# Performance work log

Measured on AMD Instinct MI355X. Metric: run time of the kernel, lower is better.

## Reference

```python
import jax, jax.numpy as jnp
import numpy as np

B, Q, H = 8, 4, 4096
NH, NKV, HD = 32, 8, 128
G = NH // NKV          # GQA group size
S = 4096               # tokens already in KV cache
CAP = S + Q            # cache capacity
SCALE = 1.0 / (HD ** 0.5)
ROPE_BASE = 10000.0


def setup_inputs() -> dict:
    key = jax.random.key(0)
    ks = jax.random.split(key, 8)
    hidden_states = jax.random.normal(ks[0], (B, Q, H), jnp.float32) * 0.02
    cache_lens = jnp.full((B,), S, dtype=jnp.int32)
    # rope tables for the new token positions [cache_len, cache_len+Q)
    pos = (cache_lens[:, None] + jnp.arange(Q)[None, :]).astype(jnp.float32)  # [B,Q]
    inv_freq = 1.0 / (ROPE_BASE ** (jnp.arange(0, HD, 2, dtype=jnp.float32) / HD))
    freqs = pos[..., None] * inv_freq[None, None, :]        # [B,Q,HD/2]
    emb = jnp.concatenate([freqs, freqs], axis=-1)          # [B,Q,HD]
    cos, sin = jnp.cos(emb), jnp.sin(emb)
    w_scale = H ** -0.5
    Wq = jax.random.normal(ks[1], (H, NH * HD), jnp.float32) * w_scale
    Wk = jax.random.normal(ks[2], (H, NKV * HD), jnp.float32) * w_scale
    Wv = jax.random.normal(ks[3], (H, NKV * HD), jnp.float32) * w_scale
    Wo = jax.random.normal(ks[4], (NH * HD, H), jnp.float32) * w_scale
    K_cache = jax.random.normal(ks[5], (B, CAP, NKV, HD), jnp.float32) * 0.02
    V_cache = jax.random.normal(ks[6], (B, CAP, NKV, HD), jnp.float32) * 0.02
    return dict(hidden_states=hidden_states, cos=cos, sin=sin,
                Wq=Wq, Wk=Wk, Wv=Wv, Wo=Wo,
                K_cache=K_cache, V_cache=V_cache, cache_lens=cache_lens)


def _rotate_half(x):
    x1, x2 = jnp.split(x, 2, axis=-1)
    return jnp.concatenate([-x2, x1], axis=-1)


def reference(hidden_states, cos, sin, Wq, Wk, Wv, Wo, K_cache, V_cache, cache_lens):
    # QKV projections (bias-free, Llama style)
    q = (hidden_states @ Wq).reshape(B, Q, NH, HD)
    k = (hidden_states @ Wk).reshape(B, Q, NKV, HD)
    v = (hidden_states @ Wv).reshape(B, Q, NKV, HD)
    # RoPE (unsqueeze_dim=2 -> broadcast over heads)
    c, s = cos[:, :, None, :], sin[:, :, None, :]
    q = q * c + _rotate_half(q) * s
    k = k * c + _rotate_half(k) * s
    # write new K/V into cache at position cache_lens (per batch)
    b_idx = jnp.arange(B)[:, None]                         # [B,1]
    w_idx = cache_lens[:, None] + jnp.arange(Q)[None, :]   # [B,Q]
    K = K_cache.at[b_idx, w_idx].set(k)                    # [B,CAP,NKV,HD]
    V = V_cache.at[b_idx, w_idx].set(v)
    # GQA attention without materializing repeated KV
    qg = q.reshape(B, Q, NKV, G, HD)
    scores = jnp.einsum('bqkgd,bskd->bkgqs', qg, K) * SCALE  # [B,NKV,G,Q,CAP]
    # causal mask: query i sees cache positions <= cache_lens + i
    j = jnp.arange(CAP)
    valid = j[None, None, :] <= (cache_lens[:, None, None] + jnp.arange(Q)[None, :, None])  # [B,Q,CAP]
    scores = jnp.where(valid[:, None, None, :, :], scores, -jnp.inf)
    p = jax.nn.softmax(scores, axis=-1)
    o = jnp.einsum('bkgqs,bskd->bqkgd', p, V).reshape(B, Q, NH * HD)
    return o @ Wo
```

## Files before the change

### kernel.cpp

```cpp
#include <hip/hip_runtime.h>
#include <hip/hip_bf16.h>

#define BB 8
#define QQ 4
#define HH 4096
#define NH 32
#define NKV 8
#define GG 4
#define HD 128
#define SS 4096
#define CAP 4100
#define ROWS 32
#define NQCOL 4096
#define NKCOL 1024
#define NTOTC 6144
#define KSPLIT 32
#define KCHUNK 128
#define SCALE 0.08838834764831845f
#define TS 128
#define NSPLIT 33
#define NEG_BIG 1e30f

__global__ __launch_bounds__(256) void gemm32_part(
    const float* __restrict__ x, const float* __restrict__ W0,
    const float* __restrict__ W1, const float* __restrict__ W2,
    int n0, int n01, int ntot, float* __restrict__ part) {
  int nblk = ntot >> 8;
  int cb = blockIdx.x % nblk;
  int kb = blockIdx.x / nblk;
  int c = (cb << 8) + threadIdx.x;
  int k0 = kb << 7;

  const float* W;
  int ldw, wc;
  if (c < n0)       { W = W0; ldw = n0;         wc = c; }
  else if (c < n01) { W = W1; ldw = n01 - n0;   wc = c - n0; }
  else              { W = W2; ldw = ntot - n01; wc = c - n01; }

  const float* wp = W + (size_t)k0 * ldw + wc;
  const float* xp = x + k0;

  float acc[ROWS];
#pragma unroll
  for (int r = 0; r < ROWS; ++r) acc[r] = 0.f;

  float w0 = wp[0], w1 = wp[ldw], w2 = wp[2 * ldw], w3 = wp[3 * ldw];
  for (int kk = 0; kk < KCHUNK; kk += 4) {
    int adv = (kk + 4 < KCHUNK) ? (ldw << 2) : 0;
    wp += adv;
    float n0r = wp[0], n1r = wp[ldw], n2r = wp[2 * ldw], n3r = wp[3 * ldw];
#pragma unroll
    for (int r = 0; r < ROWS; ++r) {
      const float4 xv = *(const float4*)(xp + (r << 12) + kk);
      acc[r] = fmaf(xv.x, w0, acc[r]);
      acc[r] = fmaf(xv.y, w1, acc[r]);
      acc[r] = fmaf(xv.z, w2, acc[r]);
      acc[r] = fmaf(xv.w, w3, acc[r]);
    }
    w0 = n0r; w1 = n1r; w2 = n2r; w3 = n3r;
  }
#pragma unroll
  for (int r = 0; r < ROWS; ++r) part[(size_t)((kb << 5) + r) * ntot + c] = acc[r];
}

__global__ __launch_bounds__(256) void rope_reduce_scatter(
    const float* __restrict__ ypart, const float* __restrict__ cosb,
    const float* __restrict__ sinb, const int* __restrict__ cache_lens,
    float* __restrict__ q_buf, float* __restrict__ K_cache,
    float* __restrict__ V_cache) {
  int idx = blockIdx.x * 256 + threadIdx.x;
  if (idx < 81920) {
    int r = idx / 2560;
    int o = idx % 2560;
    int b = r >> 2, qp = r & 3;
    int c1, d;
    bool is_q;
    if (o < 2048) {
      int h = o >> 6; d = o & 63;
      c1 = h * HD + d;
      is_q = true;
    } else {
      int ok = o - 2048;
      int kvh = ok >> 6; d = ok & 63;
      c1 = NQCOL + kvh * HD + d;
      is_q = false;
    }
    int c2 = c1 + 64;
    float s1 = 0.f, s2 = 0.f;
#pragma unroll
    for (int kb = 0; kb < KSPLIT; ++kb) {
      s1 += ypart[(size_t)((kb << 5) + r) * NTOTC + c1];
      s2 += ypart[(size_t)((kb << 5) + r) * NTOTC + c2];
    }
    float cv = cosb[(r << 7) + d];
    float sv = sinb[(r << 7) + d];
    float o1 = s1 * cv - s2 * sv;
    float o2 = s2 * cv + s1 * sv;
    if (is_q) {
      q_buf[(size_t)r * NQCOL + c1] = o1 * SCALE;
      q_buf[(size_t)r * NQCOL + c2] = o2 * SCALE;
    } else {
      int kvh = (c1 - NQCOL) >> 7;
      int pos = cache_lens[b] + qp;
      size_t base = ((size_t)(b * CAP + pos) * NKV + kvh) * HD;
      K_cache[base + d] = o1;
      K_cache[base + d + 64] = o2;
    }
  } else {
    int vi = idx - 81920;
    int r = vi >> 10;
    int cc = vi & 1023;
    int b = r >> 2, qp = r & 3;
    int c = NQCOL + NKCOL + cc;
    float s = 0.f;
#pragma unroll
    for (int kb = 0; kb < KSPLIT; ++kb)
      s += ypart[(size_t)((kb << 5) + r) * NTOTC + c];
    int kvh = cc >> 7, dd = cc & 127;
    int pos = cache_lens[b] + qp;
    V_cache[((size_t)(b * CAP + pos) * NKV + kvh) * HD + dd] = s;
  }
}

__global__ __launch_bounds__(256) void attn_partial(
    const float* __restrict__ q_buf, const float* __restrict__ K_cache,
    const float* __restrict__ V_cache, const int* __restrict__ cache_lens,
    float* __restrict__ part_o, float* __restrict__ part_m,
    float* __restrict__ part_l) {
  __shared__ __align__(16) float k_lds[64 * 128];
  __shared__ __align__(16) float q_lds[16 * 132];
  __shared__ __align__(16) float p_lds[64 * 20];
  __shared__ float ml_lds[32];
  __shared__ float alpha_lds[16];

  int g = blockIdx.x & 63;
  int split = blockIdx.x >> 6;
  int b = g >> 3, kv = g & 7;
  int t = threadIdx.x, w = t >> 6, lane = t & 63;
  int cl = cache_lens[b];
  int cl3 = cl + 3;
  int jb = split * TS;

  for (int i = t; i < 512; i += 256) {
    int qi = i >> 5, d4 = (i & 31) << 2;
    const float4 v = *(const float4*)(q_buf +
        (size_t)((b << 2) + (qi >> 2)) * NQCOL + (((kv << 2) + (qi & 3)) << 7) + d4);
    *(float4*)&q_lds[qi * 132 + d4] = v;
  }
  if (t < 16) { ml_lds[t] = -NEG_BIG; ml_lds[16 + t] = 0.f; }

  int pg = lane >> 2, dq = lane & 3;
  int dg = lane & 31, qh = lane >> 5;

  float orun[4][8];
#pragma unroll
  for (int di = 0; di < 4; ++di)
#pragma unroll
    for (int qq = 0; qq < 8; ++qq) orun[di][qq] = 0.f;

  for (int h = 0; h < 2; ++h) {
    int jbh = jb + (h << 6);

    for (int i = t; i < 2048; i += 256) {
      int r = i >> 5;
      int cbyte = (i & 31) << 4;
      int j = min(jbh + r, cl3);
      const float4 vv = *(const float4*)((const char*)K_cache +
          (((size_t)(b * CAP + j) * NKV + kv) << 9) + cbyte);
      *(float4*)((char*)k_lds + ((size_t)r << 9) + (cbyte ^ ((r & 7) << 4))) = vv;
    }
    __syncthreads();

    float acc[4][4];
#pragma unroll
    for (int i = 0; i < 4; ++i)
#pragma unroll
      for (int j = 0; j < 4; ++j) acc[i][j] = 0.f;

    for (int s = 0; s < 8; ++s) {
      int d0 = (dq << 5) + (s << 2);
      const float4 q0 = *(const float4*)&q_lds[(4 * w + 0) * 132 + d0];
      const float4 q1 = *(const float4*)&q_lds[(4 * w + 1) * 132 + d0];
      const float4 q2 = *(const float4*)&q_lds[(4 * w + 2) * 132 + d0];
      const float4 q3 = *(const float4*)&q_lds[(4 * w + 3) * 132 + d0];
#pragma unroll
      for (int i = 0; i < 4; ++i) {
        int r = pg + (i << 4);
        const float4 kk = *(const float4*)((const char*)k_lds +
            (r << 9) + ((unsigned)(d0 << 2) ^ ((r & 7) << 4)));
        acc[i][0] = fmaf(kk.x, q0.x, acc[i][0]);
        acc[i][0] = fmaf(kk.y, q0.y, acc[i][0]);
        acc[i][0] = fmaf(kk.z, q0.z, acc[i][0]);
        acc[i][0] = fmaf(kk.w, q0.w, acc[i][0]);
        acc[i][1] = fmaf(kk.x, q1.x, acc[i][1]);
        acc[i][1] = fmaf(kk.y, q1.y, acc[i][1]);
        acc[i][1] = fmaf(kk.z, q1.z, acc[i][1]);
        acc[i][1] = fmaf(kk.w, q1.w, acc[i][1]);
        acc[i][2] = fmaf(kk.x, q2.x, acc[i][2]);
        acc[i][2] = fmaf(kk.y, q2.y, acc[i][2]);
        acc[i][2] = fmaf(kk.z, q2.z, acc[i][2]);
        acc[i][2] = fmaf(kk.w, q2.w, acc[i][2]);
        acc[i][3] = fmaf(kk.x, q3.x, acc[i][3]);
        acc[i][3] = fmaf(kk.y, q3.y, acc[i][3]);
        acc[i][3] = fmaf(kk.z, q3.z, acc[i][3]);
        acc[i][3] = fmaf(kk.w, q3.w, acc[i][3]);
      }
    }

#pragma unroll
    for (int i = 0; i < 4; ++i)
#pragma unroll
      for (int j = 0; j < 4; ++j) {
        float v = acc[i][j];
        v += __shfl_xor(v, 1);
        v += __shfl_xor(v, 2);
        acc[i][j] = v;
      }

    bool okv[4];
#pragma unroll
    for (int i = 0; i < 4; ++i) {
      okv[i] = (jbh + pg + (i << 4)) <= (cl + w);
#pragma unroll
      for (int j = 0; j < 4; ++j)
        if (!okv[i]) acc[i][j] = -NEG_BIG;
    }

    float m4[4], l4[4], a4[4];
#pragma unroll
    for (int j = 0; j < 4; ++j) {
      float m = fmaxf(fmaxf(acc[0][j], acc[1][j]), fmaxf(acc[2][j], acc[3][j]));
      m = fmaxf(m, __shfl_xor(m, 4));
      m = fmaxf(m, __shfl_xor(m, 8));
      m = fmaxf(m, __shfl_xor(m, 16));
      m = fmaxf(m, __shfl_xor(m, 32));
      float mo = ml_lds[(w << 2) + j];
      float lo = ml_lds[16 + (w << 2) + j];
      float nm = fmaxf(mo, m);
      float l = 0.f;
#pragma unroll
      for (int i = 0; i < 4; ++i) {
        float e = okv[i] ? __expf(acc[i][j] - nm) : 0.f;
        acc[i][j] = e;
        l += e;
      }
      l += __shfl_xor(l, 4);
      l += __shfl_xor(l, 8);
      l += __shfl_xor(l, 16);
      l += __shfl_xor(l, 32);
      float al = __expf(mo - nm);
      m4[j] = nm; l4[j] = lo * al + l; a4[j] = al;
    }

#pragma unroll
    for (int i = 0; i < 4; ++i) {
      float pv = (dq == 0) ? acc[i][0] : (dq == 1) ? acc[i][1]
               : (dq == 2) ? acc[i][2] : acc[i][3];
      p_lds[(pg + (i << 4)) * 20 + (w << 2) + dq] = pv;
    }
    if (lane < 4) {
      float mm = (lane == 0) ? m4[0] : (lane == 1) ? m4[1] : (lane == 2) ? m4[2] : m4[3];
      float ll = (lane == 0) ? l4[0] : (lane == 1) ? l4[1] : (lane == 2) ? l4[2] : l4[3];
      float aa = (lane == 0) ? a4[0] : (lane == 1) ? a4[1] : (lane == 2) ? a4[2] : a4[3];
      ml_lds[(w << 2) + lane] = mm;
      ml_lds[16 + (w << 2) + lane] = ll;
      alpha_lds[(w << 2) + lane] = aa;
    }
    __syncthreads();

    float alq[8];
#pragma unroll
    for (int qq = 0; qq < 8; ++qq) alq[qq] = alpha_lds[(qh << 3) + qq];
#pragma unroll
    for (int di = 0; di < 4; ++di)
#pragma unroll
      for (int qq = 0; qq < 8; ++qq) orun[di][qq] *= alq[qq];

    for (int jj = 0; jj < 16; ++jj) {
      int j = (w << 4) + jj;
      int jg = min(jbh + j, cl3);
      const float4 vv = *(const float4*)(V_cache +
          (((size_t)(b * CAP + jg) * NKV + kv) << 7) + (dg << 2));
      const float4 pa = *(const float4*)&p_lds[j * 20 + (qh << 3)];
      const float4 pb = *(const float4*)&p_lds[j * 20 + (qh << 3) + 4];
      orun[0][0] = fmaf(vv.x, pa.x, orun[0][0]); orun[1][0] = fmaf(vv.y, pa.x, orun[1][0]);
      orun[2][0] = fmaf(vv.z, pa.x, orun[2][0]); orun[3][0] = fmaf(vv.w, pa.x, orun[3][0]);
      orun[0][1] = fmaf(vv.x, pa.y, orun[0][1]); orun[1][1] = fmaf(vv.y, pa.y, orun[1][1]);
      orun[2][1] = fmaf(vv.z, pa.y, orun[2][1]); orun[3][1] = fmaf(vv.w, pa.y, orun[3][1]);
      orun[0][2] = fmaf(vv.x, pa.z, orun[0][2]); orun[1][2] = fmaf(vv.y, pa.z, orun[1][2]);
      orun[2][2] = fmaf(vv.z, pa.z, orun[2][2]); orun[3][2] = fmaf(vv.w, pa.z, orun[3][2]);
      orun[0][3] = fmaf(vv.x, pa.w, orun[0][3]); orun[1][3] = fmaf(vv.y, pa.w, orun[1][3]);
      orun[2][3] = fmaf(vv.z, pa.w, orun[2][3]); orun[3][3] = fmaf(vv.w, pa.w, orun[3][3]);
      orun[0][4] = fmaf(vv.x, pb.x, orun[0][4]); orun[1][4] = fmaf(vv.y, pb.x, orun[1][4]);
      orun[2][4] = fmaf(vv.z, pb.x, orun[2][4]); orun[3][4] = fmaf(vv.w, pb.x, orun[3][4]);
      orun[0][5] = fmaf(vv.x, pb.y, orun[0][5]); orun[1][5] = fmaf(vv.y, pb.y, orun[1][5]);
      orun[2][5] = fmaf(vv.z, pb.y, orun[2][5]); orun[3][5] = fmaf(vv.w, pb.y, orun[3][5]);
      orun[0][6] = fmaf(vv.x, pb.z, orun[0][6]); orun[1][6] = fmaf(vv.y, pb.z, orun[1][6]);
      orun[2][6] = fmaf(vv.z, pb.z, orun[2][6]); orun[3][6] = fmaf(vv.w, pb.z, orun[3][6]);
      orun[0][7] = fmaf(vv.x, pb.w, orun[0][7]); orun[1][7] = fmaf(vv.y, pb.w, orun[1][7]);
      orun[2][7] = fmaf(vv.z, pb.w, orun[2][7]); orun[3][7] = fmaf(vv.w, pb.w, orun[3][7]);
    }
  }

  float* om = k_lds;
#pragma unroll
  for (int qq = 0; qq < 8; ++qq) {
    int q = (qh << 3) + qq;
    float4 ov = make_float4(orun[0][qq], orun[1][qq], orun[2][qq], orun[3][qq]);
    *(float4*)&om[(size_t)(((w << 4) + q) << 7) + (dg << 2)] = ov;
  }
  __syncthreads();

  size_t ob = (size_t)(split * 64 + g) * 2048;
  for (int i = t; i < 2048; i += 256)
    part_o[ob + i] = om[i] + om[i + 2048] + om[i + 4096] + om[i + 6144];
  if (t < 16) {
    part_m[(size_t)(split * 64 + g) * 16 + t] = ml_lds[t];
    part_l[(size_t)(split * 64 + g) * 16 + t] = ml_lds[16 + t];
  }
}

__global__ __launch_bounds__(256) void attn_combine(
    const float* __restrict__ part_o, const float* __restrict__ part_m,
    const float* __restrict__ part_l, float* __restrict__ attn_out) {
  int idx = blockIdx.x * 256 + threadIdx.x;
  int d = idx & 127;
  int qi = (idx >> 7) & 15;
  int g = idx >> 11;
  int b = g >> 3, kv = g & 7;
  float M = -NEG_BIG;
#pragma unroll 4
  for (int s = 0; s < NSPLIT; ++s) M = fmaxf(M, part_m[(size_t)(s * 64 + g) * 16 + qi]);
  float osum = 0.f, L = 0.f;
#pragma unroll 4
  for (int s = 0; s < NSPLIT; ++s) {
    size_t ml = (size_t)(s * 64 + g) * 16 + qi;
    float wgt = __expf(part_m[ml] - M);
    osum += part_o[ml * 128 + d] * wgt;
    L += part_l[ml] * wgt;
  }
  int qp = qi >> 2, gi = qi & 3;
  attn_out[(size_t)((b << 2) + qp) * NQCOL + (((kv << 2) + gi) << 7) + d] = osum / L;
}

__global__ __launch_bounds__(256) void reduce_out(
    const float* __restrict__ opart, float* __restrict__ out) {
  int idx = blockIdx.x * 256 + threadIdx.x;
  int c = idx & 4095;
  int r = idx >> 12;
  float s = 0.f;
#pragma unroll
  for (int kb = 0; kb < KSPLIT; ++kb)
    s += opart[(size_t)((kb << 5) + r) * NQCOL + c];
  out[idx] = s;
}

extern "C" void kernel_launch(void* const* d_in, const int* in_sizes, int n_in,
                              void* d_out, int out_size, void* d_ws, size_t ws_size,
                              hipStream_t stream) {
  const float* hidden = (const float*)d_in[0];
  const float* cosb   = (const float*)d_in[1];
  const float* sinb   = (const float*)d_in[2];
  const float* Wq     = (const float*)d_in[3];
  const float* Wk     = (const float*)d_in[4];
  const float* Wv     = (const float*)d_in[5];
  const float* Wo     = (const float*)d_in[6];
  float* K_cache      = (float*)d_in[7];
  float* V_cache      = (float*)d_in[8];
  const int* cache_lens = (const int*)d_in[9];
  float* out = (float*)d_out;

  const size_t BUF0 = (size_t)KSPLIT * ROWS * NTOTC;
  float* buf0     = (float*)d_ws;
  float* q_buf    = buf0 + BUF0;
  float* part_m   = q_buf + (size_t)ROWS * NQCOL;
  float* part_l   = part_m + (size_t)NSPLIT * 64 * 16;
  float* attn_out = part_l + (size_t)NSPLIT * 64 * 16;

  gemm32_part<<<(NTOTC / 256) * KSPLIT, 256, 0, stream>>>(
      hidden, Wq, Wk, Wv, NQCOL, NQCOL + NKCOL, NTOTC, buf0);
  rope_reduce_scatter<<<448, 256, 0, stream>>>(
      buf0, cosb, sinb, cache_lens, q_buf, K_cache, V_cache);
  attn_partial<<<64 * NSPLIT, 256, 0, stream>>>(
      q_buf, K_cache, V_cache, cache_lens, buf0, part_m, part_l);
  attn_combine<<<512, 256, 0, stream>>>(buf0, part_m, part_l, attn_out);
  gemm32_part<<<(NQCOL / 256) * KSPLIT, 256, 0, stream>>>(
      attn_out, Wo, Wo, Wo, NQCOL, NQCOL, NQCOL, buf0);
  reduce_out<<<512, 256, 0, stream>>>(buf0, out);
}
```

Before: 556.4 us.

## Stage activations in LDS, prefetch weights, and double-buffer K tiles in attention

```diff
diff --git a/kernel.cpp b/kernel.cpp
--- a/kernel.cpp
+++ b/kernel.cpp
@@ -6,9 +6,7 @@
 #define HH 4096
 #define NH 32
 #define NKV 8
-#define GG 4
 #define HD 128
-#define SS 4096
 #define CAP 4100
 #define ROWS 32
 #define NQCOL 4096
@@ -21,46 +19,114 @@
 #define NSPLIT 33
 #define NEG_BIG 1e30f
 
+template <bool WIDE>
 __global__ __launch_bounds__(256) void gemm32_part(
     const float* __restrict__ x, const float* __restrict__ W0,
     const float* __restrict__ W1, const float* __restrict__ W2,
     int n0, int n01, int ntot, float* __restrict__ part) {
-  int nblk = ntot >> 8;
+  __shared__ __align__(16) float x_lds[ROWS * KCHUNK];
+  const int CPB = WIDE ? 512 : 256;
+  int nblk = ntot / CPB;
   int cb = blockIdx.x % nblk;
   int kb = blockIdx.x / nblk;
-  int c = (cb << 8) + threadIdx.x;
   int k0 = kb << 7;
 
-  const float* W;
-  int ldw, wc;
+  for (int i = threadIdx.x; i < 1024; i += 256) {
+    int r = i >> 5, gq = (i & 31) << 2;
+    *(float4*)&x_lds[(r << 7) + gq] =
+        *(const float4*)(x + ((size_t)r << 12) + k0 + gq);
+  }
+  __syncthreads();
+
+  int c = cb * CPB + (WIDE ? (threadIdx.x << 1) : (int)threadIdx.x);
+  const float* W; int ldw, wc;
   if (c < n0)       { W = W0; ldw = n0;         wc = c; }
   else if (c < n01) { W = W1; ldw = n01 - n0;   wc = c - n0; }
   else              { W = W2; ldw = ntot - n01; wc = c - n01; }
-
   const float* wp = W + (size_t)k0 * ldw + wc;
-  const float* xp = x + k0;
-
-  float acc[ROWS];
-#pragma unroll
-  for (int r = 0; r < ROWS; ++r) acc[r] = 0.f;
-
-  float w0 = wp[0], w1 = wp[ldw], w2 = wp[2 * ldw], w3 = wp[3 * ldw];
-  for (int kk = 0; kk < KCHUNK; kk += 4) {
-    int adv = (kk + 4 < KCHUNK) ? (ldw << 2) : 0;
-    wp += adv;
-    float n0r = wp[0], n1r = wp[ldw], n2r = wp[2 * ldw], n3r = wp[3 * ldw];
+
+  if (WIDE) {
+    float acc[ROWS][2];
+#pragma unroll
+    for (int r = 0; r < ROWS; ++r) { acc[r][0] = 0.f; acc[r][1] = 0.f; }
+    float2 a[4], bq[4];
+#pragma unroll
+    for (int u = 0; u < 4; ++u) {
+      const float* p0 = wp + (size_t)u * ldw;
+      const float* p1 = wp + (size_t)(u + 4) * ldw;
+      a[u].x = __builtin_nontemporal_load(p0);
+      a[u].y = __builtin_nontemporal_load(p0 + 1);
+      bq[u].x = __builtin_nontemporal_load(p1);
+      bq[u].y = __builtin_nontemporal_load(p1 + 1);
+    }
+    for (int kk = 0; kk < KCHUNK; kk += 4) {
+      float2 cq[4];
+      if (kk + 8 < KCHUNK) {
+#pragma unroll
+        for (int u = 0; u < 4; ++u) {
+          const float* p = wp + (size_t)(kk + 8 + u) * ldw;
+          cq[u].x = __builtin_nontemporal_load(p);
+          cq[u].y = __builtin_nontemporal_load(p + 1);
+        }
+      } else {
+#pragma unroll
+        for (int u = 0; u < 4; ++u) cq[u] = a[u];
+      }
+#pragma unroll
+      for (int r = 0; r < ROWS; ++r) {
+        const float4 xv = *(const float4*)&x_lds[(r << 7) + kk];
+        acc[r][0] = fmaf(xv.x, a[0].x, acc[r][0]);
+        acc[r][1] = fmaf(xv.x, a[0].y, acc[r][1]);
+        acc[r][0] = fmaf(xv.y, a[1].x, acc[r][0]);
+        acc[r][1] = fmaf(xv.y, a[1].y, acc[r][1]);
+        acc[r][0] = fmaf(xv.z, a[2].x, acc[r][0]);
+        acc[r][1] = fmaf(xv.z, a[2].y, acc[r][1]);
+        acc[r][0] = fmaf(xv.w, a[3].x, acc[r][0]);
+        acc[r][1] = fmaf(xv.w, a[3].y, acc[r][1]);
+      }
+#pragma unroll
+      for (int u = 0; u < 4; ++u) { a[u] = bq[u]; bq[u] = cq[u]; }
+    }
 #pragma unroll
     for (int r = 0; r < ROWS; ++r) {
-      const float4 xv = *(const float4*)(xp + (r << 12) + kk);
-      acc[r] = fmaf(xv.x, w0, acc[r]);
-      acc[r] = fmaf(xv.y, w1, acc[r]);
-      acc[r] = fmaf(xv.z, w2, acc[r]);
-      acc[r] = fmaf(xv.w, w3, acc[r]);
-    }
-    w0 = n0r; w1 = n1r; w2 = n2r; w3 = n3r;
-  }
-#pragma unroll
-  for (int r = 0; r < ROWS; ++r) part[(size_t)((kb << 5) + r) * ntot + c] = acc[r];
+      float2 st = make_float2(acc[r][0], acc[r][1]);
+      *(float2*)(part + (size_t)((kb << 5) + r) * ntot + c) = st;
+    }
+  } else {
+    float acc[ROWS];
+#pragma unroll
+    for (int r = 0; r < ROWS; ++r) acc[r] = 0.f;
+    float a[4], bq[4];
+#pragma unroll
+    for (int u = 0; u < 4; ++u) {
+      a[u] = __builtin_nontemporal_load(wp + (size_t)u * ldw);
+      bq[u] = __builtin_nontemporal_load(wp + (size_t)(u + 4) * ldw);
+    }
+    for (int kk = 0; kk < KCHUNK; kk += 4) {
+      float cq[4];
+      if (kk + 8 < KCHUNK) {
+#pragma unroll
+        for (int u = 0; u < 4; ++u)
+          cq[u] = __builtin_nontemporal_load(wp + (size_t)(kk + 8 + u) * ldw);
+      } else {
+#pragma unroll
+        for (int u = 0; u < 4; ++u) cq[u] = a[u];
+      }
+#pragma unroll
+      for (int r = 0; r < ROWS; ++r) {
+        const float4 xv = *(const float4*)&x_lds[(r << 7) + kk];
+        acc[r] = fmaf(xv.x, a[0], acc[r]);
+        acc[r] = fmaf(xv.y, a[1], acc[r]);
+        acc[r] = fmaf(xv.z, a[2], acc[r]);
+        acc[r] = fmaf(xv.w, a[3], acc[r]);
+      }
+#pragma unroll
+      for (int u = 0; u < 4; ++u) { a[u] = bq[u]; bq[u] = cq[u]; }
+    }
+#pragma unroll
+    for (int r = 0; r < ROWS; ++r)
+      part[(size_t)((kb << 5) + r) * ntot + c] = acc[r];
+  }
 }
 
 __global__ __launch_bounds__(256) void rope_reduce_scatter(
@@ -127,9 +193,9 @@
     const float* __restrict__ V_cache, const int* __restrict__ cache_lens,
     float* __restrict__ part_o, float* __restrict__ part_m,
     float* __restrict__ part_l) {
-  __shared__ __align__(16) float k_lds[64 * 128];
-  __shared__ __align__(16) float q_lds[16 * 132];
-  __shared__ __align__(16) float p_lds[64 * 20];
+  __shared__ __align__(16) float k_lds[2][32 * 128];
+  __shared__ __align__(16) float q_lds[16 * 144];
+  __shared__ __align__(16) float p_lds[32 * 20];
   __shared__ float ml_lds[32];
   __shared__ float alpha_lds[16];
 
@@ -145,49 +211,78 @@
     int qi = i >> 5, d4 = (i & 31) << 2;
     const float4 v = *(const float4*)(q_buf +
         (size_t)((b << 2) + (qi >> 2)) * NQCOL + (((kv << 2) + (qi & 3)) << 7) + d4);
-    *(float4*)&q_lds[qi * 132 + d4] = v;
+    *(float4*)&q_lds[qi * 144 + (d4 >> 5) * 36 + (d4 & 31)] = v;
   }
   if (t < 16) { ml_lds[t] = -NEG_BIG; ml_lds[16 + t] = 0.f; }
 
   int pg = lane >> 2, dq = lane & 3;
   int dg = lane & 31, qh = lane >> 5;
 
+  float4 kreg[4];
+#pragma unroll
+  for (int u = 0; u < 4; ++u) {
+    int i = t + (u << 8);
+    int r = i >> 5, gk = i & 31;
+    int j = min(jb + r, cl3);
+    kreg[u] = *(const float4*)((const char*)K_cache +
+        (((size_t)(b * CAP + j) * NKV + kv) << 9) + (gk << 4));
+  }
+#pragma unroll
+  for (int u = 0; u < 4; ++u) {
+    int i = t + (u << 8);
+    int r = i >> 5, gk = i & 31;
+    *(float4*)((char*)&k_lds[0][0] + (r << 9) + ((gk << 4) ^ ((r & 7) << 4))) = kreg[u];
+  }
+  __syncthreads();
+
   float orun[4][8];
 #pragma unroll
   for (int di = 0; di < 4; ++di)
 #pragma unroll
     for (int qq = 0; qq < 8; ++qq) orun[di][qq] = 0.f;
 
-  for (int h = 0; h < 2; ++h) {
-    int jbh = jb + (h << 6);
-
-    for (int i = t; i < 2048; i += 256) {
-      int r = i >> 5;
-      int cbyte = (i & 31) << 4;
-      int j = min(jbh + r, cl3);
-      const float4 vv = *(const float4*)((const char*)K_cache +
-          (((size_t)(b * CAP + j) * NKV + kv) << 9) + cbyte);
-      *(float4*)((char*)k_lds + ((size_t)r << 9) + (cbyte ^ ((r & 7) << 4))) = vv;
-    }
-    __syncthreads();
-
-    float acc[4][4];
-#pragma unroll
-    for (int i = 0; i < 4; ++i)
+  int cur = 0;
+  for (int st = 0; st < 4; ++st) {
+    int jbh = jb + (st << 5);
+
+    float4 vreg[8];
+#pragma unroll
+    for (int jj = 0; jj < 8; ++jj) {
+      int j = min(jbh + (w << 3) + jj, cl3);
+      vreg[jj] = *(const float4*)(V_cache +
+          (((size_t)(b * CAP + j) * NKV + kv) << 7) + (dg << 2));
+    }
+    bool have_next = (st < 3);
+    if (have_next) {
+      int jbn = jbh + 32;
+#pragma unroll
+      for (int u = 0; u < 4; ++u) {
+        int i = t + (u << 8);
+        int r = i >> 5, gk = i & 31;
+        int j = min(jbn + r, cl3);
+        kreg[u] = *(const float4*)((const char*)K_cache +
+            (((size_t)(b * CAP + j) * NKV + kv) << 9) + (gk << 4));
+      }
+    }
+
+    const float* kl = &k_lds[cur][0];
+    float acc[2][4];
+#pragma unroll
+    for (int i = 0; i < 2; ++i)
 #pragma unroll
       for (int j = 0; j < 4; ++j) acc[i][j] = 0.f;
 
     for (int s = 0; s < 8; ++s) {
-      int d0 = (dq << 5) + (s << 2);
-      const float4 q0 = *(const float4*)&q_lds[(4 * w + 0) * 132 + d0];
-      const float4 q1 = *(const float4*)&q_lds[(4 * w + 1) * 132 + d0];
-      const float4 q2 = *(const float4*)&q_lds[(4 * w + 2) * 132 + d0];
-      const float4 q3 = *(const float4*)&q_lds[(4 * w + 3) * 132 + d0];
-#pragma unroll
-      for (int i = 0; i < 4; ++i) {
+      int qoff = dq * 36 + (s << 2);
+      const float4 q0 = *(const float4*)&q_lds[(4 * w + 0) * 144 + qoff];
+      const float4 q1 = *(const float4*)&q_lds[(4 * w + 1) * 144 + qoff];
+      const float4 q2 = *(const float4*)&q_lds[(4 * w + 2) * 144 + qoff];
+      const float4 q3 = *(const float4*)&q_lds[(4 * w + 3) * 144 + qoff];
+#pragma unroll
+      for (int i = 0; i < 2; ++i) {
         int r = pg + (i << 4);
-        const float4 kk = *(const float4*)((const char*)k_lds +
-            (r << 9) + ((unsigned)(d0 << 2) ^ ((r & 7) << 4)));
+        const float4 kk = *(const float4*)((const char*)kl +
+            (r << 9) + ((unsigned)((dq << 7) | (s << 4)) ^ ((r & 7) << 4)));
         acc[i][0] = fmaf(kk.x, q0.x, acc[i][0]);
         acc[i][0] = fmaf(kk.y, q0.y, acc[i][0]);
         acc[i][0] = fmaf(kk.z, q0.z, acc[i][0]);
@@ -208,7 +303,7 @@
     }
 
 #pragma unroll
-    for (int i = 0; i < 4; ++i)
+    for (int i = 0; i < 2; ++i)
 #pragma unroll
       for (int j = 0; j < 4; ++j) {
         float v = acc[i][j];
@@ -217,9 +312,9 @@
         acc[i][j] = v;
       }
 
-    bool okv[4];
-#pragma unroll
-    for (int i = 0; i < 4; ++i) {
+    bool okv[2];
+#pragma unroll
+    for (int i = 0; i < 2; ++i) {
       okv[i] = (jbh + pg + (i << 4)) <= (cl + w);
 #pragma unroll
       for (int j = 0; j < 4; ++j)
@@ -229,7 +324,7 @@
     float m4[4], l4[4], a4[4];
 #pragma unroll
     for (int j = 0; j < 4; ++j) {
-      float m = fmaxf(fmaxf(acc[0][j], acc[1][j]), fmaxf(acc[2][j], acc[3][j]));
+      float m = fmaxf(acc[0][j], acc[1][j]);
       m = fmaxf(m, __shfl_xor(m, 4));
       m = fmaxf(m, __shfl_xor(m, 8));
       m = fmaxf(m, __shfl_xor(m, 16));
@@ -239,7 +334,7 @@
       float nm = fmaxf(mo, m);
       float l = 0.f;
 #pragma unroll
-      for (int i = 0; i < 4; ++i) {
+      for (int i = 0; i < 2; ++i) {
         float e = okv[i] ? __expf(acc[i][j] - nm) : 0.f;
         acc[i][j] = e;
         l += e;
@@ -253,7 +348,7 @@
     }
 
 #pragma unroll
-    for (int i = 0; i < 4; ++i) {
+    for (int i = 0; i < 2; ++i) {
       float pv = (dq == 0) ? acc[i][0] : (dq == 1) ? acc[i][1]
                : (dq == 2) ? acc[i][2] : acc[i][3];
       p_lds[(pg + (i << 4)) * 20 + (w << 2) + dq] = pv;
@@ -266,6 +361,15 @@
       ml_lds[16 + (w << 2) + lane] = ll;
       alpha_lds[(w << 2) + lane] = aa;
     }
+    if (have_next) {
+      char* dst = (char*)&k_lds[cur ^ 1][0];
+#pragma unroll
+      for (int u = 0; u < 4; ++u) {
+        int i = t + (u << 8);
+        int r = i >> 5, gk = i & 31;
+        *(float4*)(dst + (r << 9) + ((gk << 4) ^ ((r & 7) << 4))) = kreg[u];
+      }
+    }
     __syncthreads();
 
     float alq[8];
@@ -276,11 +380,10 @@
 #pragma unroll
       for (int qq = 0; qq < 8; ++qq) orun[di][qq] *= alq[qq];
 
-    for (int jj = 0; jj < 16; ++jj) {
-      int j = (w << 4) + jj;
-      int jg = min(jbh + j, cl3);
-      const float4 vv = *(const float4*)(V_cache +
-          (((size_t)(b * CAP + jg) * NKV + kv) << 7) + (dg << 2));
+#pragma unroll
+    for (int jj = 0; jj < 8; ++jj) {
+      int j = (w << 3) + jj;
+      const float4 vv = vreg[jj];
       const float4 pa = *(const float4*)&p_lds[j * 20 + (qh << 3)];
       const float4 pb = *(const float4*)&p_lds[j * 20 + (qh << 3) + 4];
       orun[0][0] = fmaf(vv.x, pa.x, orun[0][0]); orun[1][0] = fmaf(vv.y, pa.x, orun[1][0]);
@@ -300,9 +403,11 @@
       orun[0][7] = fmaf(vv.x, pb.w, orun[0][7]); orun[1][7] = fmaf(vv.y, pb.w, orun[1][7]);
       orun[2][7] = fmaf(vv.z, pb.w, orun[2][7]); orun[3][7] = fmaf(vv.w, pb.w, orun[3][7]);
     }
-  }
-
-  float* om = k_lds;
+    cur ^= 1;
+    __syncthreads();
+  }
+
+  float* om = &k_lds[0][0];
 #pragma unroll
   for (int qq = 0; qq < 8; ++qq) {
     int q = (qh << 3) + qq;
@@ -377,14 +482,14 @@
   float* part_l   = part_m + (size_t)NSPLIT * 64 * 16;
   float* attn_out = part_l + (size_t)NSPLIT * 64 * 16;
 
-  gemm32_part<<<(NTOTC / 256) * KSPLIT, 256, 0, stream>>>(
+  gemm32_part<true><<<(NTOTC / 512) * KSPLIT, 256, 0, stream>>>(
       hidden, Wq, Wk, Wv, NQCOL, NQCOL + NKCOL, NTOTC, buf0);
   rope_reduce_scatter<<<448, 256, 0, stream>>>(
       buf0, cosb, sinb, cache_lens, q_buf, K_cache, V_cache);
   attn_partial<<<64 * NSPLIT, 256, 0, stream>>>(
       q_buf, K_cache, V_cache, cache_lens, buf0, part_m, part_l);
   attn_combine<<<512, 256, 0, stream>>>(buf0, part_m, part_l, attn_out);
-  gemm32_part<<<(NQCOL / 256) * KSPLIT, 256, 0, stream>>>(
+  gemm32_part<false><<<(NQCOL / 256) * KSPLIT, 256, 0, stream>>>(
       attn_out, Wo, Wo, Wo, NQCOL, NQCOL, NQCOL, buf0);
   reduce_out<<<512, 256, 0, stream>>>(buf0, out);
 }
```

New measurement: 490.9 us. 11.8% less time.
